# Kernel tuning notes

Hardware: AMD Instinct MI355X
Metric: run time of the kernel (lower is better)

Reference implementation:

```python
import jax, jax.numpy as jnp
import numpy as np

D_MODEL = 1024
NUM_HEADS = 16
HEAD_SIZE = D_MODEL // NUM_HEADS  # 64; used ONLY as the softmax scale (module never splits heads)


def setup_inputs() -> dict:
    key = jax.random.key(0)
    ks = jax.random.split(key, 7)
    B, L, D = 4, 2048, D_MODEL
    q = jax.random.normal(ks[0], (B, L, D), dtype=jnp.float32)
    k = jax.random.normal(ks[1], (B, L, D), dtype=jnp.float32)
    v = jax.random.normal(ks[2], (B, L, D), dtype=jnp.float32)
    s = 1.0 / np.sqrt(D)
    Wq = jax.random.uniform(ks[3], (D, D), jnp.float32, -s, s)
    Wk = jax.random.uniform(ks[4], (D, D), jnp.float32, -s, s)
    Wv = jax.random.uniform(ks[5], (D, D), jnp.float32, -s, s)
    Wproj = jax.random.uniform(ks[6], (D, D), jnp.float32, -s, s)
    return {"q": q, "k": k, "v": v, "Wq": Wq, "Wk": Wk, "Wv": Wv, "Wproj": Wproj}


def reference(q, k, v, Wq, Wk, Wv, Wproj):
    # nn.Linear(x) = x @ W.T; weights stored [out, in]
    L = q.shape[1]
    qh = jnp.einsum('bld,ed->ble', q, Wq)
    kh = jnp.einsum('bld,ed->ble', k, Wk)
    vh = jnp.einsum('bld,ed->ble', v, Wv)
    # NOTE: module attends over the full d_model channel (no head split),
    # but scales by head_size ** -0.5 — faithful to the source.
    att = jnp.einsum('bqd,bkd->bqk', qh, kh) * (HEAD_SIZE ** -0.5)
    causal = jnp.tril(jnp.ones((L, L), dtype=bool))  # bias buffer
    att = jnp.where(causal, att, -jnp.inf)
    att = jax.nn.softmax(att, axis=-1)
    y = jnp.einsum('bqk,bkd->bqd', att, vh)
    y = jnp.einsum('bld,ed->ble', y, Wproj)
    return y
```

## Files before the change

### kernel.cpp

```cpp
#include <hip/hip_runtime.h>
#include <hip/hip_bf16.h>
#include <stdint.h>

typedef __bf16 bf16x8 __attribute__((ext_vector_type(8)));
typedef float  f32x4  __attribute__((ext_vector_type(4)));
typedef unsigned short ushort8v __attribute__((ext_vector_type(8)));

__device__ __forceinline__ unsigned short f2bf(float f) {
  unsigned int u = __float_as_uint(f);
  u += 0x7FFF + ((u >> 16) & 1);
  return (unsigned short)(u >> 16);
}

#define BM 128
#define BN 128
#define BK 32

#define GLOAD_LDS(gptr, ldsptr)                                                     \
  __builtin_amdgcn_global_load_lds(                                                 \
      (const __attribute__((address_space(1))) unsigned int*)(gptr),                \
      (__attribute__((address_space(3))) unsigned int*)(ldsptr), 16, 0, 0)

__global__ __launch_bounds__(256, 3) void gemm_bt(
    const unsigned short* __restrict__ A,
    const unsigned short* __restrict__ B,
    void* __restrict__ C,
    int M, int N, int K, int ntiles,
    long sAz, long sBz, long sCz,
    int mode, int causal_skip, int klimit, float scale)
{
  const int nwg  = gridDim.x;
  const int orig = blockIdx.x;
  const int qq = nwg >> 3, rr = nwg & 7, xc = orig & 7, oo = orig >> 3;
  const int wg = (xc < rr ? xc * (qq + 1) : rr * (qq + 1) + (xc - rr) * qq) + oo;
  const int mt = wg / ntiles, nt = wg % ntiles;
  const int z  = blockIdx.y;
  if (causal_skip && nt > mt) return;
  const int emode = (mode == 3) ? (z == 2 ? 1 : 0) : mode;

  A += sAz * (long)z;
  B += sBz * (long)z;

  __shared__ __align__(16) unsigned short As[3][BM * BK];
  __shared__ __align__(16) unsigned short Bs[3][BN * BK];

  const int tid  = threadIdx.x;
  const int wave = tid >> 6;
  const int lane = tid & 63;
  const int wr = wave >> 1, wc = wave & 1;

  f32x4 acc[4][4];
#pragma unroll
  for (int i = 0; i < 4; ++i)
#pragma unroll
    for (int j = 0; j < 4; ++j) acc[i][j] = (f32x4){0.f, 0.f, 0.f, 0.f};

  int kiters = K / BK;
  if (klimit) { int kl = (mt + 1) * BM; if (kl < K) kiters = kl / BK; }

  const int r0 = tid >> 2, s0 = tid & 3;
  const int c0 = ((s0 ^ ((r0 >> 1) & 3)) << 3);
  const int r1 = r0 + 64;
  const int c1 = ((s0 ^ ((r1 >> 1) & 3)) << 3);
  const long aoff0 = (long)(mt * BM + r0) * K + c0;
  const long aoff1 = (long)(mt * BM + r1) * K + c1;
  const long boff0 = (long)(nt * BN + r0) * K + c0;
  const long boff1 = (long)(nt * BN + r1) * K + c1;
  const unsigned ldsw = wave * 1024;

#define STAGE(bi, k0)                                                     \
  do {                                                                    \
    GLOAD_LDS(A + aoff0 + (k0), (char*)&As[bi][0]    + ldsw);             \
    GLOAD_LDS(A + aoff1 + (k0), (char*)&As[bi][2048] + ldsw);             \
    GLOAD_LDS(B + boff0 + (k0), (char*)&Bs[bi][0]    + ldsw);             \
    GLOAD_LDS(B + boff1 + (k0), (char*)&Bs[bi][2048] + ldsw);             \
  } while (0)

  STAGE(0, 0);
  if (kiters > 1) STAGE(1, BK);

  int cur = 0;
  for (int kt = 0; kt < kiters; ++kt) {
    const int rem = kiters - 1 - kt;
    if (rem >= 2) {
      int sb = cur + 2; if (sb >= 3) sb -= 3;
      STAGE(sb, (kt + 2) * BK);
      asm volatile("s_waitcnt vmcnt(8)" ::: "memory");
    } else if (rem == 1) {
      asm volatile("s_waitcnt vmcnt(4)" ::: "memory");
    } else {
      asm volatile("s_waitcnt vmcnt(0)" ::: "memory");
    }
    __builtin_amdgcn_s_barrier();
    asm volatile("" ::: "memory");

    bf16x8 af[4], bfr[4];
#pragma unroll
    for (int i = 0; i < 4; ++i) {
      const int ar = wr * 64 + i * 16 + (lane & 15);
      const int as = ((lane >> 4) ^ ((ar >> 1) & 3)) << 3;
      af[i] = *(const bf16x8*)&As[cur][ar * BK + as];
      const int br = wc * 64 + i * 16 + (lane & 15);
      const int bs = ((lane >> 4) ^ ((br >> 1) & 3)) << 3;
      bfr[i] = *(const bf16x8*)&Bs[cur][br * BK + bs];
    }
#pragma unroll
    for (int mi = 0; mi < 4; ++mi)
#pragma unroll
      for (int ni = 0; ni < 4; ++ni)
        acc[mi][ni] = __builtin_amdgcn_mfma_f32_16x16x32_bf16(af[mi], bfr[ni], acc[mi][ni], 0, 0, 0);

    asm volatile("" ::: "memory");
    __builtin_amdgcn_s_barrier();
    cur = (cur == 2) ? 0 : cur + 1;
  }
#undef STAGE

  const int rb = mt * BM + wr * 64;
  const int cb = nt * BN + wc * 64;

  if (emode == 0) {
    unsigned short* Cb = (unsigned short*)C + sCz * (long)z;
#pragma unroll
    for (int mi = 0; mi < 4; ++mi)
#pragma unroll
      for (int ni = 0; ni < 4; ++ni) {
        const int row0 = rb + mi * 16 + ((lane >> 4) << 2);
        const int col  = cb + ni * 16 + (lane & 15);
#pragma unroll
        for (int j = 0; j < 4; ++j)
          Cb[(long)(row0 + j) * N + col] = f2bf(acc[mi][ni][j]);
      }
  } else if (emode == 1) {
    unsigned short* Cb = (unsigned short*)C + sCz * (long)z;
#pragma unroll
    for (int mi = 0; mi < 4; ++mi)
#pragma unroll
      for (int ni = 0; ni < 4; ++ni) {
        const int row0 = rb + mi * 16 + ((lane >> 4) << 2);
        const int col  = cb + ni * 16 + (lane & 15);
#pragma unroll
        for (int j = 0; j < 4; ++j) {
          const int row = row0 + j;
          const int b = row >> 11, l = row & 2047;
          Cb[((long)b * N + col) * 2048 + l] = f2bf(acc[mi][ni][j]);
        }
      }
  } else {
    float* Cf = (float*)C + sCz * (long)z;
#pragma unroll
    for (int mi = 0; mi < 4; ++mi)
#pragma unroll
      for (int ni = 0; ni < 4; ++ni) {
        const int row0 = rb + mi * 16 + ((lane >> 4) << 2);
        const int col  = cb + ni * 16 + (lane & 15);
#pragma unroll
        for (int j = 0; j < 4; ++j)
          Cf[(long)(row0 + j) * N + col] = acc[mi][ni][j] * scale;
      }
  }
}

__global__ __launch_bounds__(256) void convert_all(
    const float* __restrict__ q, const float* __restrict__ k, const float* __restrict__ v,
    const float* __restrict__ wq, const float* __restrict__ wk,
    const float* __restrict__ wv, const float* __restrict__ wp,
    unsigned short* __restrict__ qkv, unsigned short* __restrict__ wb)
{
  const long NQ = 8192L * 1024 / 4;
  const long NW = 1024L * 1024 / 4;
  const int blk = blockIdx.x;
  const float* src; unsigned short* dst; long n; int nb, bb;
  if (blk < 1536) {
    const int s = blk >> 9;
    src = (s == 0) ? q : (s == 1) ? k : v;
    dst = qkv + (long)s * (8192L * 1024);
    n = NQ; nb = 512; bb = blk & 511;
  } else {
    const int s = (blk - 1536) >> 6;
    src = (s == 0) ? wq : (s == 1) ? wk : (s == 2) ? wv : wp;
    dst = wb + (long)s * (1024L * 1024);
    n = NW; nb = 64; bb = (blk - 1536) & 63;
  }
  for (long i = (long)bb * 256 + threadIdx.x; i < n; i += (long)nb * 256) {
    float4 x = ((const float4*)src)[i];
    ushort4 o;
    o.x = f2bf(x.x); o.y = f2bf(x.y); o.z = f2bf(x.z); o.w = f2bf(x.w);
    ((ushort4*)dst)[i] = o;
  }
}

__global__ __launch_bounds__(256) void softmax_causal(
    const float* __restrict__ S, unsigned short* __restrict__ P, int L)
{
  const int r = blockIdx.x;
  const int b = r >> 11, q = r & 2047;
  const float* srow = S + ((long)b * L + q) * L;
  unsigned short* prow = P + ((long)b * L + q) * L;
  const int len = q + 1;
  const int tid = threadIdx.x, lane = tid & 63, wave = tid >> 6;
  const int base = tid * 8;
  __shared__ float red[8];

  float4 x0 = ((const float4*)srow)[tid * 2];
  float4 x1 = ((const float4*)srow)[tid * 2 + 1];
  float vv[8] = {x0.x, x0.y, x0.z, x0.w, x1.x, x1.y, x1.z, x1.w};

  float m = -3.4e38f;
#pragma unroll
  for (int i = 0; i < 8; ++i) if (base + i < len) m = fmaxf(m, vv[i]);
#pragma unroll
  for (int o = 32; o; o >>= 1) m = fmaxf(m, __shfl_xor(m, o));
  if (lane == 0) red[wave] = m;
  __syncthreads();
  m = fmaxf(fmaxf(red[0], red[1]), fmaxf(red[2], red[3]));

  float p[8], s = 0.f;
#pragma unroll
  for (int i = 0; i < 8; ++i) {
    p[i] = (base + i < len) ? __expf(vv[i] - m) : 0.f;
    s += p[i];
  }
#pragma unroll
  for (int o = 32; o; o >>= 1) s += __shfl_xor(s, o);
  if (lane == 0) red[4 + wave] = s;
  __syncthreads();
  s = (red[4] + red[5]) + (red[6] + red[7]);
  const float inv = 1.f / s;

  ushort8v o16;
#pragma unroll
  for (int i = 0; i < 8; ++i) o16[i] = f2bf(p[i] * inv);
  *(ushort8v*)(prow + base) = o16;
}

extern "C" void kernel_launch(void* const* d_in, const int* in_sizes, int n_in,
                              void* d_out, int out_size, void* d_ws, size_t ws_size,
                              hipStream_t stream) {
  const float* q  = (const float*)d_in[0];
  const float* k  = (const float*)d_in[1];
  const float* v  = (const float*)d_in[2];
  const float* Wq = (const float*)d_in[3];
  const float* Wk = (const float*)d_in[4];
  const float* Wv = (const float*)d_in[5];
  const float* Wp = (const float*)d_in[6];
  float* out = (float*)d_out;

  const long D    = 1024;
  const long L    = 2048;
  const long ND   = 8192 * D;
  const long NS   = 4L * L * L;

  char* ws = (char*)d_ws;
  unsigned short* qh    = (unsigned short*)ws;
  unsigned short* kh    = qh  + ND;
  unsigned short* vhT   = kh  + ND;
  unsigned short* P     = vhT + ND;
  unsigned short* ybf   = P   + NS;
  unsigned short* wbf   = ybf + ND;
  float*          S     = (float*)(wbf + 4L * D * D);
  unsigned short* qkvbf = (unsigned short*)S;

  convert_all<<<1792, 256, 0, stream>>>(q, k, v, Wq, Wk, Wv, Wp, qkvbf, wbf);

  gemm_bt<<<dim3(512, 3), 256, 0, stream>>>(qkvbf, wbf, qh,
      8192, 1024, 1024, 8, ND, D * D, ND, 3, 0, 0, 1.0f);

  gemm_bt<<<dim3(256, 4), 256, 0, stream>>>(qh, kh, S,
      2048, 2048, 1024, 16, L * D, L * D, L * L, 2, 1, 0, 0.125f);

  softmax_causal<<<8192, 256, 0, stream>>>(S, P, 2048);

  gemm_bt<<<dim3(128, 4), 256, 0, stream>>>(P, vhT, ybf,
      2048, 1024, 2048, 8, L * L, D * L, L * D, 0, 0, 1, 1.0f);

  gemm_bt<<<dim3(512, 1), 256, 0, stream>>>(ybf, wbf + 3 * D * D, out,
      8192, 1024, 1024, 8, 0, 0, 0, 2, 0, 0, 1.0f);
}
```

Before: 238.2 us.

## Add 256x256-tile 8-wave GEMM with interleaved LDS staging for QKV and QK^T

Adds a new GEMM kernel that uses 256x256 output tiles with 512 threads, a 64-wide K step split into halves, double-buffered direct global-to-LDS loads interleaved with MFMA phases, and s_setprio around the MFMA blocks. The QKV projection and the causal QK^T score GEMM now use this kernel, which is meant to raise arithmetic intensity and overlap loads with compute. The old kernel loses its transposed-store mode because it is no longer needed. Larger tiles mean fewer workgroups and coarser causal skipping on the diagonal, and they raise register and LDS pressure (128KB of LDS per block).

Result: no change. 234.0 us (-1.8%).

```diff
diff --git a/kernel.cpp b/kernel.cpp
--- a/kernel.cpp
+++ b/kernel.cpp
@@ -12,14 +12,191 @@
   return (unsigned short)(u >> 16);
 }
 
-#define BM 128
-#define BN 128
-#define BK 32
-
 #define GLOAD_LDS(gptr, ldsptr)                                                     \
   __builtin_amdgcn_global_load_lds(                                                 \
       (const __attribute__((address_space(1))) unsigned int*)(gptr),                \
       (__attribute__((address_space(3))) unsigned int*)(ldsptr), 16, 0, 0)
+
+__global__ __launch_bounds__(512, 2) void gemm256(
+    const unsigned short* __restrict__ A,
+    const unsigned short* __restrict__ B,
+    void* __restrict__ C,
+    int M, int N, int K, int ntn,
+    long sAz, long sBz, long sCz,
+    int mode, int causal_skip, float scale)
+{
+  const int nwg = gridDim.x, orig = blockIdx.x;
+  const int qq = nwg >> 3, rr = nwg & 7, xcd = orig & 7, oo = orig >> 3;
+  const int wg = (xcd < rr ? xcd * (qq + 1) : rr * (qq + 1) + (xcd - rr) * qq) + oo;
+  const int mt = wg / ntn, nt = wg % ntn;
+  const int z = blockIdx.y;
+  if (causal_skip && nt > mt) return;
+  const int emode = (mode == 3) ? (z == 2 ? 1 : 0) : mode;
+  A += sAz * (long)z;
+  B += sBz * (long)z;
+
+  __shared__ __align__(16) unsigned short lds[65536];
+
+  const int tid  = threadIdx.x;
+  const int wave = tid >> 6;
+  const int lane = tid & 63;
+  const int wr = wave >> 2, wc = wave & 3;
+  const int li = lane & 15;
+  const int psw16 = (((lane >> 4) ^ ((lane >> 1) & 3)) << 4);
+
+  f32x4 acc[8][4];
+#pragma unroll
+  for (int i = 0; i < 8; ++i)
+#pragma unroll
+    for (int jn = 0; jn < 4; ++jn) acc[i][jn] = (f32x4){0.f, 0.f, 0.f, 0.f};
+
+  const int nkt = K / 64;
+
+  const int srow = tid >> 2;
+  const long scol = (long)(((tid & 3) ^ ((tid >> 3) & 3)) << 3);
+  const long gA0 = (long)(mt * 256 + srow) * K + scol;
+  const long gA1 = (long)(mt * 256 + 128 + srow) * K + scol;
+  const long gB0 = (long)(nt * 256 + srow) * K + scol;
+  const long gB1 = (long)(nt * 256 + 128 + srow) * K + scol;
+  const int stw0 = wave * 1024;
+  const int stw1 = 8192 + wave * 1024;
+
+#define ABASE(c, kh) ((((c) * 2 + (kh)) * 16384))
+#define BBASE(c, kh) ((65536 + ((c) * 2 + (kh)) * 16384))
+#define STAGE_A(kt, kh) do { const long o = (long)(kt) * 64 + (kh) * 32;            \
+    GLOAD_LDS(A + gA0 + o, (char*)lds + ABASE((kt) & 1, kh) + stw0);                \
+    GLOAD_LDS(A + gA1 + o, (char*)lds + ABASE((kt) & 1, kh) + stw1); } while (0)
+#define STAGE_B(kt, kh) do { const long o = (long)(kt) * 64 + (kh) * 32;            \
+    GLOAD_LDS(B + gB0 + o, (char*)lds + BBASE((kt) & 1, kh) + stw0);                \
+    GLOAD_LDS(B + gB1 + o, (char*)lds + BBASE((kt) & 1, kh) + stw1); } while (0)
+#define RD_A(c, kk, mset, mf) \
+  (*(const bf16x8*)((const char*)lds + ABASE(c, kk) + (wr * 128 + (mset) * 64 + (mf) * 16 + li) * 64 + psw16))
+#define RD_B(c, kk, nf) \
+  (*(const bf16x8*)((const char*)lds + BBASE(c, kk) + (wc * 64 + (nf) * 16 + li) * 64 + psw16))
+
+  STAGE_B(0, 0); STAGE_A(0, 0); STAGE_B(0, 1); STAGE_A(0, 1);
+  STAGE_B(1, 0); STAGE_A(1, 0); STAGE_B(1, 1);
+  asm volatile("s_waitcnt vmcnt(6)" ::: "memory");
+  __builtin_amdgcn_s_barrier();
+
+  bf16x8 a[4], b0[4], b1[4];
+  for (int j = 0; j < nkt; ++j) {
+    const int c = j & 1;
+
+#pragma unroll
+    for (int nf = 0; nf < 4; ++nf) b0[nf] = RD_B(c, 0, nf);
+#pragma unroll
+    for (int mf = 0; mf < 4; ++mf) a[mf] = RD_A(c, 0, 0, mf);
+    if (j + 1 < nkt) STAGE_A(j + 1, 1);
+    __builtin_amdgcn_s_barrier();
+    __builtin_amdgcn_s_setprio(1);
+#pragma unroll
+    for (int mf = 0; mf < 4; ++mf)
+#pragma unroll
+      for (int nf = 0; nf < 4; ++nf)
+        acc[mf][nf] = __builtin_amdgcn_mfma_f32_16x16x32_bf16(a[mf], b0[nf], acc[mf][nf], 0, 0, 0);
+    __builtin_amdgcn_s_setprio(0);
+    __builtin_amdgcn_s_barrier();
+
+#pragma unroll
+    for (int mf = 0; mf < 4; ++mf) a[mf] = RD_A(c, 0, 1, mf);
+    if (j + 2 < nkt) STAGE_B(j + 2, 0);
+    __builtin_amdgcn_s_barrier();
+    __builtin_amdgcn_s_setprio(1);
+#pragma unroll
+    for (int mf = 0; mf < 4; ++mf)
+#pragma unroll
+      for (int nf = 0; nf < 4; ++nf)
+        acc[4 + mf][nf] = __builtin_amdgcn_mfma_f32_16x16x32_bf16(a[mf], b0[nf], acc[4 + mf][nf], 0, 0, 0);
+    __builtin_amdgcn_s_setprio(0);
+    __builtin_amdgcn_s_barrier();
+
+#pragma unroll
+    for (int nf = 0; nf < 4; ++nf) b1[nf] = RD_B(c, 1, nf);
+#pragma unroll
+    for (int mf = 0; mf < 4; ++mf) a[mf] = RD_A(c, 1, 0, mf);
+    if (j + 2 < nkt) STAGE_A(j + 2, 0);
+    __builtin_amdgcn_s_barrier();
+    __builtin_amdgcn_s_setprio(1);
+#pragma unroll
+    for (int mf = 0; mf < 4; ++mf)
+#pragma unroll
+      for (int nf = 0; nf < 4; ++nf)
+        acc[mf][nf] = __builtin_amdgcn_mfma_f32_16x16x32_bf16(a[mf], b1[nf], acc[mf][nf], 0, 0, 0);
+    __builtin_amdgcn_s_setprio(0);
+    __builtin_amdgcn_s_barrier();
+
+#pragma unroll
+    for (int mf = 0; mf < 4; ++mf) a[mf] = RD_A(c, 1, 1, mf);
+    if (j + 2 < nkt) STAGE_B(j + 2, 1);
+    __builtin_amdgcn_s_barrier();
+    __builtin_amdgcn_s_setprio(1);
+#pragma unroll
+    for (int mf = 0; mf < 4; ++mf)
+#pragma unroll
+      for (int nf = 0; nf < 4; ++nf)
+        acc[4 + mf][nf] = __builtin_amdgcn_mfma_f32_16x16x32_bf16(a[mf], b1[nf], acc[4 + mf][nf], 0, 0, 0);
+    __builtin_amdgcn_s_setprio(0);
+    if (j + 1 < nkt) {
+      if (j + 2 < nkt) { asm volatile("s_waitcnt vmcnt(6)" ::: "memory"); }
+      else             { asm volatile("s_waitcnt vmcnt(0)" ::: "memory"); }
+    }
+    __builtin_amdgcn_s_barrier();
+  }
+#undef ABASE
+#undef BBASE
+#undef STAGE_A
+#undef STAGE_B
+#undef RD_A
+#undef RD_B
+
+  const int rb = mt * 256 + wr * 128;
+  const int cb = nt * 256 + wc * 64;
+  if (emode == 0) {
+    unsigned short* Cb = (unsigned short*)C + sCz * (long)z;
+#pragma unroll
+    for (int mi = 0; mi < 8; ++mi)
+#pragma unroll
+      for (int ni = 0; ni < 4; ++ni) {
+        const int row0 = rb + mi * 16 + ((lane >> 4) << 2);
+        const int col  = cb + ni * 16 + (lane & 15);
+#pragma unroll
+        for (int jj = 0; jj < 4; ++jj)
+          Cb[(long)(row0 + jj) * N + col] = f2bf(acc[mi][ni][jj]);
+      }
+  } else if (emode == 1) {
+    unsigned short* Cb = (unsigned short*)C + sCz * (long)z;
+#pragma unroll
+    for (int mi = 0; mi < 8; ++mi)
+#pragma unroll
+      for (int ni = 0; ni < 4; ++ni) {
+        const int row0 = rb + mi * 16 + ((lane >> 4) << 2);
+        const int col  = cb + ni * 16 + (lane & 15);
+#pragma unroll
+        for (int jj = 0; jj < 4; ++jj) {
+          const int row = row0 + jj;
+          const int b = row >> 11, l = row & 2047;
+          Cb[((long)b * N + col) * 2048 + l] = f2bf(acc[mi][ni][jj]);
+        }
+      }
+  } else {
+    float* Cf = (float*)C + sCz * (long)z;
+#pragma unroll
+    for (int mi = 0; mi < 8; ++mi)
+#pragma unroll
+      for (int ni = 0; ni < 4; ++ni) {
+        const int row0 = rb + mi * 16 + ((lane >> 4) << 2);
+        const int col  = cb + ni * 16 + (lane & 15);
+#pragma unroll
+        for (int jj = 0; jj < 4; ++jj)
+          Cf[(long)(row0 + jj) * N + col] = acc[mi][ni][jj] * scale;
+      }
+  }
+}
+
+#define BM 128
+#define BN 128
+#define BK 32
 
 __global__ __launch_bounds__(256, 3) void gemm_bt(
     const unsigned short* __restrict__ A,
@@ -36,7 +213,6 @@
   const int mt = wg / ntiles, nt = wg % ntiles;
   const int z  = blockIdx.y;
   if (causal_skip && nt > mt) return;
-  const int emode = (mode == 3) ? (z == 2 ? 1 : 0) : mode;
 
   A += sAz * (long)z;
   B += sBz * (long)z;
@@ -119,7 +295,7 @@
   const int rb = mt * BM + wr * 64;
   const int cb = nt * BN + wc * 64;
 
-  if (emode == 0) {
+  if (mode == 0) {
     unsigned short* Cb = (unsigned short*)C + sCz * (long)z;
 #pragma unroll
     for (int mi = 0; mi < 4; ++mi)
@@ -130,21 +306,6 @@
 #pragma unroll
         for (int j = 0; j < 4; ++j)
           Cb[(long)(row0 + j) * N + col] = f2bf(acc[mi][ni][j]);
-      }
-  } else if (emode == 1) {
-    unsigned short* Cb = (unsigned short*)C + sCz * (long)z;
-#pragma unroll
-    for (int mi = 0; mi < 4; ++mi)
-#pragma unroll
-      for (int ni = 0; ni < 4; ++ni) {
-        const int row0 = rb + mi * 16 + ((lane >> 4) << 2);
-        const int col  = cb + ni * 16 + (lane & 15);
-#pragma unroll
-        for (int j = 0; j < 4; ++j) {
-          const int row = row0 + j;
-          const int b = row >> 11, l = row & 2047;
-          Cb[((long)b * N + col) * 2048 + l] = f2bf(acc[mi][ni][j]);
-        }
       }
   } else {
     float* Cf = (float*)C + sCz * (long)z;
@@ -263,11 +424,11 @@
 
   convert_all<<<1792, 256, 0, stream>>>(q, k, v, Wq, Wk, Wv, Wp, qkvbf, wbf);
 
-  gemm_bt<<<dim3(512, 3), 256, 0, stream>>>(qkvbf, wbf, qh,
-      8192, 1024, 1024, 8, ND, D * D, ND, 3, 0, 0, 1.0f);
-
-  gemm_bt<<<dim3(256, 4), 256, 0, stream>>>(qh, kh, S,
-      2048, 2048, 1024, 16, L * D, L * D, L * L, 2, 1, 0, 0.125f);
+  gemm256<<<dim3(128, 3), 512, 0, stream>>>(qkvbf, wbf, qh,
+      8192, 1024, 1024, 4, ND, D * D, ND, 3, 0, 1.0f);
+
+  gemm256<<<dim3(64, 4), 512, 0, stream>>>(qh, kh, S,
+      2048, 2048, 1024, 8, L * D, L * D, L * L, 2, 1, 0.125f);
 
   softmax_causal<<<8192, 256, 0, stream>>>(S, P, 2048);
 
```

## Fuse softmax normalization into PV GEMM and launch only causal QK tiles

Applied to the files above, without the earlier changes.

The separate softmax kernel that wrote a bf16 P matrix is replaced. A lightweight rowstats kernel now computes only the per-row max and inverse sum. A new pv_fused GEMM reads fp32 scores, applies exp, scaling and the causal mask while staging A into LDS, and multiplies by V. The QK GEMM now launches only the 136 lower-triangular tiles, using a triangular index map, instead of launching 256 and early-exiting. This removes the P write and read traffic and the wasted blocks. In exchange, the PV loop reads fp32 scores (twice the bytes of bf16), recomputes exp inline, and uses a shallower two-stage register-staged pipeline.

After: 279.9 us. 17.5% more time.

```diff
diff --git a/kernel.cpp b/kernel.cpp
--- a/kernel.cpp
+++ b/kernel.cpp
@@ -12,14 +12,14 @@
   return (unsigned short)(u >> 16);
 }
 
-#define BM 128
-#define BN 128
-#define BK 32
-
 #define GLOAD_LDS(gptr, ldsptr)                                                     \
   __builtin_amdgcn_global_load_lds(                                                 \
       (const __attribute__((address_space(1))) unsigned int*)(gptr),                \
       (__attribute__((address_space(3))) unsigned int*)(ldsptr), 16, 0, 0)
+
+#define BM 128
+#define BN 128
+#define BK 32
 
 __global__ __launch_bounds__(256, 3) void gemm_bt(
     const unsigned short* __restrict__ A,
@@ -27,15 +27,23 @@
     void* __restrict__ C,
     int M, int N, int K, int ntiles,
     long sAz, long sBz, long sCz,
-    int mode, int causal_skip, int klimit, float scale)
+    int mode, int tilemap, float scale)
 {
-  const int nwg  = gridDim.x;
+  int mt, nt;
   const int orig = blockIdx.x;
-  const int qq = nwg >> 3, rr = nwg & 7, xc = orig & 7, oo = orig >> 3;
-  const int wg = (xc < rr ? xc * (qq + 1) : rr * (qq + 1) + (xc - rr) * qq) + oo;
-  const int mt = wg / ntiles, nt = wg % ntiles;
-  const int z  = blockIdx.y;
-  if (causal_skip && nt > mt) return;
+  if (tilemap == 0) {
+    const int nwg = gridDim.x;
+    const int qq = nwg >> 3, rr = nwg & 7, xc = orig & 7, oo = orig >> 3;
+    const int wg = (xc < rr ? xc * (qq + 1) : rr * (qq + 1) + (xc - rr) * qq) + oo;
+    mt = wg / ntiles; nt = wg % ntiles;
+  } else {
+    mt = (int)((sqrtf(8.f * orig + 1.f) - 1.f) * 0.5f);
+    int base = mt * (mt + 1) / 2;
+    if (orig < base) { mt--; base = mt * (mt + 1) / 2; }
+    else if (orig >= base + mt + 1) { mt++; base = mt * (mt + 1) / 2; }
+    nt = orig - base;
+  }
+  const int z = blockIdx.y;
   const int emode = (mode == 3) ? (z == 2 ? 1 : 0) : mode;
 
   A += sAz * (long)z;
@@ -55,8 +63,7 @@
 #pragma unroll
     for (int j = 0; j < 4; ++j) acc[i][j] = (f32x4){0.f, 0.f, 0.f, 0.f};
 
-  int kiters = K / BK;
-  if (klimit) { int kl = (mt + 1) * BM; if (kl < K) kiters = kl / BK; }
+  const int kiters = K / BK;
 
   const int r0 = tid >> 2, s0 = tid & 3;
   const int c0 = ((s0 ^ ((r0 >> 1) & 3)) << 3);
@@ -159,6 +166,165 @@
           Cf[(long)(row0 + j) * N + col] = acc[mi][ni][j] * scale;
       }
   }
+}
+
+__global__ __launch_bounds__(256, 3) void pv_fused(
+    const float* __restrict__ S, const float2* __restrict__ stats,
+    const unsigned short* __restrict__ vhT, unsigned short* __restrict__ Y)
+{
+  const int orig = blockIdx.x;
+  const int z = blockIdx.y;
+  const int mt = (orig & 8) ? (15 - (orig & 7)) : (orig & 7);
+  const int nt = orig >> 4;
+  const float* Sb = S + (long)z * (2048L * 2048);
+  const float2* st = stats + (long)z * 2048;
+  const unsigned short* Bb = vhT + (long)z * (1024L * 2048);
+  unsigned short* Yb = Y + (long)z * (2048L * 1024);
+
+  __shared__ __align__(16) unsigned short As[2][128 * 32];
+  __shared__ __align__(16) unsigned short Bs[2][128 * 32];
+
+  const int tid = threadIdx.x, wave = tid >> 6, lane = tid & 63;
+  const int wr = wave >> 1, wc = wave & 1;
+
+  f32x4 acc[4][4];
+#pragma unroll
+  for (int i = 0; i < 4; ++i)
+#pragma unroll
+    for (int j = 0; j < 4; ++j) acc[i][j] = (f32x4){0.f, 0.f, 0.f, 0.f};
+
+  const int kiters = (mt + 1) * 4;
+
+  const int arow = tid >> 1;
+  const int q = mt * 128 + arow;
+  const float2 ms = st[q];
+  const float* srow = Sb + (long)q * 2048;
+  const int acs = (tid & 1) * 2;
+  const int asw = (arow >> 1) & 3;
+  unsigned short* wp0a = &As[0][arow * 32 + (acs ^ asw) * 8];
+  unsigned short* wp1a = &As[0][arow * 32 + ((acs + 1) ^ asw) * 8];
+  unsigned short* wp0b = &As[1][arow * 32 + (acs ^ asw) * 8];
+  unsigned short* wp1b = &As[1][arow * 32 + ((acs + 1) ^ asw) * 8];
+
+  const int r0 = tid >> 2, s0 = tid & 3;
+  const int bc0 = ((s0 ^ ((r0 >> 1) & 3)) << 3);
+  const int r1 = r0 + 64;
+  const int bc1 = ((s0 ^ ((r1 >> 1) & 3)) << 3);
+  const long boff0 = (long)(nt * 128 + r0) * 2048 + bc0;
+  const long boff1 = (long)(nt * 128 + r1) * 2048 + bc1;
+  const unsigned ldsw = wave * 1024;
+
+  float4 av0, av1, av2, av3;
+
+#define ISSUE_A(k0) do { const float4* sp = (const float4*)(srow + (k0) + acs * 8); \
+    av0 = sp[0]; av1 = sp[1]; av2 = sp[2]; av3 = sp[3]; } while (0)
+#define ISSUE_B(bi, k0) do {                                              \
+    GLOAD_LDS(Bb + boff0 + (k0), (char*)&Bs[bi][0]    + ldsw);            \
+    GLOAD_LDS(Bb + boff1 + (k0), (char*)&Bs[bi][2048] + ldsw); } while (0)
+#define EXPWRITE(sel, k0) do {                                            \
+    float pv_[16] = {av0.x, av0.y, av0.z, av0.w, av1.x, av1.y, av1.z, av1.w, \
+                     av2.x, av2.y, av2.z, av2.w, av3.x, av3.y, av3.z, av3.w}; \
+    ushort8v h0_, h1_;                                                    \
+    _Pragma("unroll")                                                     \
+    for (int i_ = 0; i_ < 8; ++i_) {                                      \
+      const int col_ = (k0) + acs * 8 + i_;                               \
+      h0_[i_] = (col_ <= q) ? f2bf(__expf(pv_[i_] - ms.x) * ms.y) : (unsigned short)0; } \
+    _Pragma("unroll")                                                     \
+    for (int i_ = 0; i_ < 8; ++i_) {                                      \
+      const int col_ = (k0) + acs * 8 + 8 + i_;                           \
+      h1_[i_] = (col_ <= q) ? f2bf(__expf(pv_[8 + i_] - ms.x) * ms.y) : (unsigned short)0; } \
+    if (sel) { *(ushort8v*)wp0b = h0_; *(ushort8v*)wp1b = h1_; }          \
+    else     { *(ushort8v*)wp0a = h0_; *(ushort8v*)wp1a = h1_; }          \
+  } while (0)
+
+  ISSUE_A(0); ISSUE_B(0, 0);
+  asm volatile("s_waitcnt vmcnt(0)" ::: "memory");
+  EXPWRITE(0, 0);
+  asm volatile("s_waitcnt lgkmcnt(0)" ::: "memory");
+  __builtin_amdgcn_s_barrier();
+  asm volatile("" ::: "memory");
+
+  int cur = 0;
+  for (int kt = 0; kt < kiters; ++kt) {
+    const int k0n = (kt + 1) * 32;
+    const bool more = (kt + 1 < kiters);
+    if (more) { ISSUE_A(k0n); ISSUE_B(cur ^ 1, k0n); }
+
+    bf16x8 af[4], bfr[4];
+#pragma unroll
+    for (int i = 0; i < 4; ++i) {
+      const int ar = wr * 64 + i * 16 + (lane & 15);
+      const int as = ((lane >> 4) ^ ((ar >> 1) & 3)) << 3;
+      af[i] = *(const bf16x8*)&As[cur][ar * 32 + as];
+      const int br = wc * 64 + i * 16 + (lane & 15);
+      const int bs = ((lane >> 4) ^ ((br >> 1) & 3)) << 3;
+      bfr[i] = *(const bf16x8*)&Bs[cur][br * 32 + bs];
+    }
+#pragma unroll
+    for (int mi = 0; mi < 4; ++mi)
+#pragma unroll
+      for (int ni = 0; ni < 4; ++ni)
+        acc[mi][ni] = __builtin_amdgcn_mfma_f32_16x16x32_bf16(af[mi], bfr[ni], acc[mi][ni], 0, 0, 0);
+
+    asm volatile("s_waitcnt vmcnt(0)" ::: "memory");
+    if (more) EXPWRITE(cur ^ 1, k0n);
+    asm volatile("s_waitcnt lgkmcnt(0)" ::: "memory");
+    __builtin_amdgcn_s_barrier();
+    asm volatile("" ::: "memory");
+    cur ^= 1;
+  }
+#undef ISSUE_A
+#undef ISSUE_B
+#undef EXPWRITE
+
+  const int rb = mt * 128 + wr * 64;
+  const int cb = nt * 128 + wc * 64;
+#pragma unroll
+  for (int mi = 0; mi < 4; ++mi)
+#pragma unroll
+    for (int ni = 0; ni < 4; ++ni) {
+      const int row0 = rb + mi * 16 + ((lane >> 4) << 2);
+      const int col  = cb + ni * 16 + (lane & 15);
+#pragma unroll
+      for (int j = 0; j < 4; ++j)
+        Yb[(long)(row0 + j) * 1024 + col] = f2bf(acc[mi][ni][j]);
+    }
+}
+
+__global__ __launch_bounds__(256) void rowstats(
+    const float* __restrict__ S, float2* __restrict__ st)
+{
+  const int r = blockIdx.x;
+  const int b = r >> 11, q = r & 2047;
+  const float* srow = S + ((long)b * 2048 + q) * 2048;
+  const int len = q + 1;
+  const int tid = threadIdx.x, lane = tid & 63, wave = tid >> 6;
+  const int base = tid * 8;
+  __shared__ float red[8];
+
+  float4 x0 = ((const float4*)srow)[tid * 2];
+  float4 x1 = ((const float4*)srow)[tid * 2 + 1];
+  float vv[8] = {x0.x, x0.y, x0.z, x0.w, x1.x, x1.y, x1.z, x1.w};
+
+  float m = -3.4e38f;
+#pragma unroll
+  for (int i = 0; i < 8; ++i) if (base + i < len) m = fmaxf(m, vv[i]);
+#pragma unroll
+  for (int o = 32; o; o >>= 1) m = fmaxf(m, __shfl_xor(m, o));
+  if (lane == 0) red[wave] = m;
+  __syncthreads();
+  m = fmaxf(fmaxf(red[0], red[1]), fmaxf(red[2], red[3]));
+
+  float s = 0.f;
+#pragma unroll
+  for (int i = 0; i < 8; ++i) if (base + i < len) s += __expf(vv[i] - m);
+#pragma unroll
+  for (int o = 32; o; o >>= 1) s += __shfl_xor(s, o);
+  if (lane == 0) red[4 + wave] = s;
+  __syncthreads();
+  s = (red[4] + red[5]) + (red[6] + red[7]);
+
+  if (tid == 0) st[r] = (float2){m, 1.f / s};
 }
 
 __global__ __launch_bounds__(256) void convert_all(
@@ -190,50 +356,6 @@
   }
 }
 
-__global__ __launch_bounds__(256) void softmax_causal(
-    const float* __restrict__ S, unsigned short* __restrict__ P, int L)
-{
-  const int r = blockIdx.x;
-  const int b = r >> 11, q = r & 2047;
-  const float* srow = S + ((long)b * L + q) * L;
-  unsigned short* prow = P + ((long)b * L + q) * L;
-  const int len = q + 1;
-  const int tid = threadIdx.x, lane = tid & 63, wave = tid >> 6;
-  const int base = tid * 8;
-  __shared__ float red[8];
-
-  float4 x0 = ((const float4*)srow)[tid * 2];
-  float4 x1 = ((const float4*)srow)[tid * 2 + 1];
-  float vv[8] = {x0.x, x0.y, x0.z, x0.w, x1.x, x1.y, x1.z, x1.w};
-
-  float m = -3.4e38f;
-#pragma unroll
-  for (int i = 0; i < 8; ++i) if (base + i < len) m = fmaxf(m, vv[i]);
-#pragma unroll
-  for (int o = 32; o; o >>= 1) m = fmaxf(m, __shfl_xor(m, o));
-  if (lane == 0) red[wave] = m;
-  __syncthreads();
-  m = fmaxf(fmaxf(red[0], red[1]), fmaxf(red[2], red[3]));
-
-  float p[8], s = 0.f;
-#pragma unroll
-  for (int i = 0; i < 8; ++i) {
-    p[i] = (base + i < len) ? __expf(vv[i] - m) : 0.f;
-    s += p[i];
-  }
-#pragma unroll
-  for (int o = 32; o; o >>= 1) s += __shfl_xor(s, o);
-  if (lane == 0) red[4 + wave] = s;
-  __syncthreads();
-  s = (red[4] + red[5]) + (red[6] + red[7]);
-  const float inv = 1.f / s;
-
-  ushort8v o16;
-#pragma unroll
-  for (int i = 0; i < 8; ++i) o16[i] = f2bf(p[i] * inv);
-  *(ushort8v*)(prow + base) = o16;
-}
-
 extern "C" void kernel_launch(void* const* d_in, const int* in_sizes, int n_in,
                               void* d_out, int out_size, void* d_ws, size_t ws_size,
                               hipStream_t stream) {
@@ -246,34 +368,32 @@
   const float* Wp = (const float*)d_in[6];
   float* out = (float*)d_out;
 
-  const long D    = 1024;
-  const long L    = 2048;
-  const long ND   = 8192 * D;
-  const long NS   = 4L * L * L;
+  const long D  = 1024;
+  const long L  = 2048;
+  const long ND = 8192 * D;
 
   char* ws = (char*)d_ws;
   unsigned short* qh    = (unsigned short*)ws;
   unsigned short* kh    = qh  + ND;
   unsigned short* vhT   = kh  + ND;
-  unsigned short* P     = vhT + ND;
-  unsigned short* ybf   = P   + NS;
+  unsigned short* ybf   = vhT + ND;
   unsigned short* wbf   = ybf + ND;
   float*          S     = (float*)(wbf + 4L * D * D);
+  float2*         stats = (float2*)(S + 4L * L * L);
   unsigned short* qkvbf = (unsigned short*)S;
 
   convert_all<<<1792, 256, 0, stream>>>(q, k, v, Wq, Wk, Wv, Wp, qkvbf, wbf);
 
   gemm_bt<<<dim3(512, 3), 256, 0, stream>>>(qkvbf, wbf, qh,
-      8192, 1024, 1024, 8, ND, D * D, ND, 3, 0, 0, 1.0f);
-
-  gemm_bt<<<dim3(256, 4), 256, 0, stream>>>(qh, kh, S,
-      2048, 2048, 1024, 16, L * D, L * D, L * L, 2, 1, 0, 0.125f);
-
-  softmax_causal<<<8192, 256, 0, stream>>>(S, P, 2048);
-
-  gemm_bt<<<dim3(128, 4), 256, 0, stream>>>(P, vhT, ybf,
-      2048, 1024, 2048, 8, L * L, D * L, L * D, 0, 0, 1, 1.0f);
+      8192, 1024, 1024, 8, ND, D * D, ND, 3, 0, 1.0f);
+
+  gemm_bt<<<dim3(136, 4), 256, 0, stream>>>(qh, kh, S,
+      2048, 2048, 1024, 16, L * D, L * D, L * L, 2, 1, 0.125f);
+
+  rowstats<<<8192, 256, 0, stream>>>(S, stats);
+
+  pv_fused<<<dim3(128, 4), 256, 0, stream>>>(S, stats, vhT, ybf);
 
   gemm_bt<<<dim3(512, 1), 256, 0, stream>>>(ybf, wbf + 3 * D * D, out,
-      8192, 1024, 1024, 8, 0, 0, 0, 2, 0, 0, 1.0f);
-}
+      8192, 1024, 1024, 8, 0, 0, 0, 2, 0, 1.0f);
+}
```

## Launch only lower-triangle QK tiles, balance PV tiles, trim softmax reads

Applied to the files above, without the earlier changes.

QK^T now launches exactly 136 lower-triangular tiles per batch, mapped through a triangular-number inverse, so no blocks start and then exit early. The PV GEMM uses a new tile order that pairs short and long causal rows (mt and 15-mt) to balance the k-limited work across blocks. Softmax only reads and writes up to the 128-aligned causal extent, skipping the masked upper region that the PV GEMM never reads. The sqrt-based index mapping adds a little arithmetic and depends on exact float behaviour, with correction steps to guard the rounding.

New measurement: 221.0 us. 7.2% less time.

```diff
diff --git a/kernel.cpp b/kernel.cpp
--- a/kernel.cpp
+++ b/kernel.cpp
@@ -12,14 +12,14 @@
   return (unsigned short)(u >> 16);
 }
 
-#define BM 128
-#define BN 128
-#define BK 32
-
 #define GLOAD_LDS(gptr, ldsptr)                                                     \
   __builtin_amdgcn_global_load_lds(                                                 \
       (const __attribute__((address_space(1))) unsigned int*)(gptr),                \
       (__attribute__((address_space(3))) unsigned int*)(ldsptr), 16, 0, 0)
+
+#define BM 128
+#define BN 128
+#define BK 32
 
 __global__ __launch_bounds__(256, 3) void gemm_bt(
     const unsigned short* __restrict__ A,
@@ -27,15 +27,27 @@
     void* __restrict__ C,
     int M, int N, int K, int ntiles,
     long sAz, long sBz, long sCz,
-    int mode, int causal_skip, int klimit, float scale)
+    int mode, int tilemap, float scale)
 {
-  const int nwg  = gridDim.x;
+  int mt, nt;
   const int orig = blockIdx.x;
-  const int qq = nwg >> 3, rr = nwg & 7, xc = orig & 7, oo = orig >> 3;
-  const int wg = (xc < rr ? xc * (qq + 1) : rr * (qq + 1) + (xc - rr) * qq) + oo;
-  const int mt = wg / ntiles, nt = wg % ntiles;
-  const int z  = blockIdx.y;
-  if (causal_skip && nt > mt) return;
+  if (tilemap == 0) {
+    const int nwg = gridDim.x;
+    const int qq = nwg >> 3, rr = nwg & 7, xc = orig & 7, oo = orig >> 3;
+    const int wg = (xc < rr ? xc * (qq + 1) : rr * (qq + 1) + (xc - rr) * qq) + oo;
+    mt = wg / ntiles; nt = wg % ntiles;
+  } else if (tilemap == 1) {
+    mt = (int)((sqrtf(8.f * orig + 1.f) - 1.f) * 0.5f);
+    int base = mt * (mt + 1) / 2;
+    if (orig < base) { mt--; base = mt * (mt + 1) / 2; }
+    else if (orig >= base + mt + 1) { mt++; base = mt * (mt + 1) / 2; }
+    nt = orig - base;
+  } else {
+    const int c = orig & 15;
+    mt = (c & 8) ? (15 - (c & 7)) : c;
+    nt = orig >> 4;
+  }
+  const int z = blockIdx.y;
   const int emode = (mode == 3) ? (z == 2 ? 1 : 0) : mode;
 
   A += sAz * (long)z;
@@ -56,7 +68,7 @@
     for (int j = 0; j < 4; ++j) acc[i][j] = (f32x4){0.f, 0.f, 0.f, 0.f};
 
   int kiters = K / BK;
-  if (klimit) { int kl = (mt + 1) * BM; if (kl < K) kiters = kl / BK; }
+  if (tilemap == 2) { const int kl = (mt + 1) * (BM / BK); if (kl < kiters) kiters = kl; }
 
   const int r0 = tid >> 2, s0 = tid & 3;
   const int c0 = ((s0 ^ ((r0 >> 1) & 3)) << 3);
@@ -158,6 +170,60 @@
         for (int j = 0; j < 4; ++j)
           Cf[(long)(row0 + j) * N + col] = acc[mi][ni][j] * scale;
       }
+  }
+}
+
+__global__ __launch_bounds__(256) void softmax_causal(
+    const float* __restrict__ S, unsigned short* __restrict__ P, int L)
+{
+  const int r = blockIdx.x;
+  const int b = r >> 11, q = r & 2047;
+  const float* srow = S + ((long)b * L + q) * L;
+  unsigned short* prow = P + ((long)b * L + q) * L;
+  const int len = q + 1;
+  const int lenceil = ((q >> 7) + 1) << 7;
+  const int tid = threadIdx.x, lane = tid & 63, wave = tid >> 6;
+  const int base = tid * 8;
+  const bool active = base < lenceil;
+  __shared__ float red[8];
+
+  float vv[8];
+#pragma unroll
+  for (int i = 0; i < 8; ++i) vv[i] = -3.4e38f;
+  if (active) {
+    float4 x0 = ((const float4*)srow)[tid * 2];
+    float4 x1 = ((const float4*)srow)[tid * 2 + 1];
+    vv[0] = x0.x; vv[1] = x0.y; vv[2] = x0.z; vv[3] = x0.w;
+    vv[4] = x1.x; vv[5] = x1.y; vv[6] = x1.z; vv[7] = x1.w;
+  }
+
+  float m = -3.4e38f;
+#pragma unroll
+  for (int i = 0; i < 8; ++i) if (base + i < len) m = fmaxf(m, vv[i]);
+#pragma unroll
+  for (int o = 32; o; o >>= 1) m = fmaxf(m, __shfl_xor(m, o));
+  if (lane == 0) red[wave] = m;
+  __syncthreads();
+  m = fmaxf(fmaxf(red[0], red[1]), fmaxf(red[2], red[3]));
+
+  float p[8], s = 0.f;
+#pragma unroll
+  for (int i = 0; i < 8; ++i) {
+    p[i] = (base + i < len) ? __expf(vv[i] - m) : 0.f;
+    s += p[i];
+  }
+#pragma unroll
+  for (int o = 32; o; o >>= 1) s += __shfl_xor(s, o);
+  if (lane == 0) red[4 + wave] = s;
+  __syncthreads();
+  s = (red[4] + red[5]) + (red[6] + red[7]);
+  const float inv = 1.f / s;
+
+  if (active) {
+    ushort8v o16;
+#pragma unroll
+    for (int i = 0; i < 8; ++i) o16[i] = f2bf(p[i] * inv);
+    *(ushort8v*)(prow + base) = o16;
   }
 }
 
@@ -190,50 +256,6 @@
   }
 }
 
-__global__ __launch_bounds__(256) void softmax_causal(
-    const float* __restrict__ S, unsigned short* __restrict__ P, int L)
-{
-  const int r = blockIdx.x;
-  const int b = r >> 11, q = r & 2047;
-  const float* srow = S + ((long)b * L + q) * L;
-  unsigned short* prow = P + ((long)b * L + q) * L;
-  const int len = q + 1;
-  const int tid = threadIdx.x, lane = tid & 63, wave = tid >> 6;
-  const int base = tid * 8;
-  __shared__ float red[8];
-
-  float4 x0 = ((const float4*)srow)[tid * 2];
-  float4 x1 = ((const float4*)srow)[tid * 2 + 1];
-  float vv[8] = {x0.x, x0.y, x0.z, x0.w, x1.x, x1.y, x1.z, x1.w};
-
-  float m = -3.4e38f;
-#pragma unroll
-  for (int i = 0; i < 8; ++i) if (base + i < len) m = fmaxf(m, vv[i]);
-#pragma unroll
-  for (int o = 32; o; o >>= 1) m = fmaxf(m, __shfl_xor(m, o));
-  if (lane == 0) red[wave] = m;
-  __syncthreads();
-  m = fmaxf(fmaxf(red[0], red[1]), fmaxf(red[2], red[3]));
-
-  float p[8], s = 0.f;
-#pragma unroll
-  for (int i = 0; i < 8; ++i) {
-    p[i] = (base + i < len) ? __expf(vv[i] - m) : 0.f;
-    s += p[i];
-  }
-#pragma unroll
-  for (int o = 32; o; o >>= 1) s += __shfl_xor(s, o);
-  if (lane == 0) red[4 + wave] = s;
-  __syncthreads();
-  s = (red[4] + red[5]) + (red[6] + red[7]);
-  const float inv = 1.f / s;
-
-  ushort8v o16;
-#pragma unroll
-  for (int i = 0; i < 8; ++i) o16[i] = f2bf(p[i] * inv);
-  *(ushort8v*)(prow + base) = o16;
-}
-
 extern "C" void kernel_launch(void* const* d_in, const int* in_sizes, int n_in,
                               void* d_out, int out_size, void* d_ws, size_t ws_size,
                               hipStream_t stream) {
@@ -246,10 +268,10 @@
   const float* Wp = (const float*)d_in[6];
   float* out = (float*)d_out;
 
-  const long D    = 1024;
-  const long L    = 2048;
-  const long ND   = 8192 * D;
-  const long NS   = 4L * L * L;
+  const long D  = 1024;
+  const long L  = 2048;
+  const long ND = 8192 * D;
+  const long NS = 4L * L * L;
 
   char* ws = (char*)d_ws;
   unsigned short* qh    = (unsigned short*)ws;
@@ -264,16 +286,16 @@
   convert_all<<<1792, 256, 0, stream>>>(q, k, v, Wq, Wk, Wv, Wp, qkvbf, wbf);
 
   gemm_bt<<<dim3(512, 3), 256, 0, stream>>>(qkvbf, wbf, qh,
-      8192, 1024, 1024, 8, ND, D * D, ND, 3, 0, 0, 1.0f);
-
-  gemm_bt<<<dim3(256, 4), 256, 0, stream>>>(qh, kh, S,
-      2048, 2048, 1024, 16, L * D, L * D, L * L, 2, 1, 0, 0.125f);
+      8192, 1024, 1024, 8, ND, D * D, ND, 3, 0, 1.0f);
+
+  gemm_bt<<<dim3(136, 4), 256, 0, stream>>>(qh, kh, S,
+      2048, 2048, 1024, 16, L * D, L * D, L * L, 2, 1, 0.125f);
 
   softmax_causal<<<8192, 256, 0, stream>>>(S, P, 2048);
 
   gemm_bt<<<dim3(128, 4), 256, 0, stream>>>(P, vhT, ybf,
-      2048, 1024, 2048, 8, L * L, D * L, L * D, 0, 0, 1, 1.0f);
+      2048, 1024, 2048, 8, L * L, D * L, L * D, 0, 2, 1.0f);
 
   gemm_bt<<<dim3(512, 1), 256, 0, stream>>>(ybf, wbf + 3 * D * D, out,
-      8192, 1024, 1024, 8, 0, 0, 0, 2, 0, 0, 1.0f);
-}
+      8192, 1024, 1024, 8, 0, 0, 0, 2, 0, 1.0f);
+}
```
